# Performance work log

Hardware: AMD Instinct MI355X
Metric: run time of the kernel (lower is better)

The kernel has to match this reference:

```python
import jax, jax.numpy as jnp
import numpy as np


def setup_inputs() -> dict:
    key = jax.random.key(0)
    kq, kk, kv = jax.random.split(key, 3)
    B, S, D = 4, 4096, 128
    q = jax.random.normal(kq, (B, S, D), dtype=jnp.float32)
    k = jax.random.normal(kk, (B, S, D), dtype=jnp.float32)
    v = jax.random.normal(kv, (B, S, D), dtype=jnp.float32)
    return {"q": q, "k": k, "v": v}


def reference(q, k, v):
    # naive scaled dot-product attention: softmax(q k^T / sqrt(d)) v
    scale = 1.0 / jnp.sqrt(jnp.asarray(q.shape[-1], q.dtype))
    scores = jnp.einsum("bsd,btd->bst", q, k) * scale  # [B,S,S]
    probs = jax.nn.softmax(scores, axis=-1)
    out = jnp.einsum("bst,btd->bsd", probs, v)  # [B,S,Dv]
    return out
```

## Files before the change

kernel.cpp:

```cpp
#include <hip/hip_runtime.h>
#include <cmath>
#include <cstdint>

typedef __attribute__((ext_vector_type(8))) __bf16 bf16x8;
typedef __attribute__((ext_vector_type(16))) float f32x16;
typedef unsigned int u32;
typedef unsigned short u16;

constexpr int Bn = 4, Sn = 4096, Dn = 128;
constexpr int OSTR = 132;
constexpr float SCL2E = 0.08838834764831845f * 1.4426950408889634f;

#if __has_builtin(__builtin_amdgcn_exp2f)
#define EXP2F(x) __builtin_amdgcn_exp2f(x)
#else
#define EXP2F(x) exp2f(x)
#endif

__device__ __forceinline__ u32 pk2(float a, float b) {
  u32 r;
  asm("v_cvt_pk_bf16_f32 %0, %1, %2" : "=v"(r) : "v"(a), "v"(b));
  return r;
}

__device__ __forceinline__ void pl32swap(u32& a, u32& b) {
  asm("v_permlane32_swap_b32 %0, %1" : "+v"(a), "+v"(b));
}

__device__ __forceinline__ void gload_lds16(const void* g, void* l) {
  __builtin_amdgcn_global_load_lds(
      (const __attribute__((address_space(1))) u32*)g,
      (__attribute__((address_space(3))) u32*)l, 16, 0, 0);
}

__launch_bounds__(256)
__global__ void prep_kv(const float* __restrict__ Kg, const float* __restrict__ Vg,
                        u16* __restrict__ Kf, u16* __restrict__ Vf) {
  __shared__ float Tl[64 * 132];
  const int kt = blockIdx.x, kind = blockIdx.y, b = blockIdx.z;
  const int tid = threadIdx.x;
  const size_t tileBase = ((size_t)b * 64 + kt) * 1024;
  const float* src = (kind == 0 ? Kg : Vg) + ((size_t)b * Sn + kt * 64) * Dn;

  #pragma unroll
  for (int r = 0; r < 8; ++r) {
    const int idx = tid + r * 256;
    const int row = idx >> 5, col = (idx & 31) * 4;
    float4 v = *(const float4*)(src + (size_t)row * Dn + col);
    *(float4*)(Tl + row * 132 + col) = v;
  }
  __syncthreads();
  if (kind == 0) {
    #pragma unroll
    for (int r = 0; r < 4; ++r) {
      const int g = tid + r * 256;
      const int c = g & 31, h = (g >> 5) & 1, tile = (g >> 6) & 1, kc = g >> 7;
      const float* s = Tl + (tile * 32 + c) * 132 + kc * 16 + h * 8;
      float4 f0 = *(const float4*)(s);
      float4 f1 = *(const float4*)(s + 4);
      uint4 o;
      o.x = pk2(f0.x, f0.y); o.y = pk2(f0.z, f0.w);
      o.z = pk2(f1.x, f1.y); o.w = pk2(f1.z, f1.w);
      *(uint4*)(Kf + (tileBase + g) * 8) = o;
    }
  } else {
    #pragma unroll
    for (int r = 0; r < 4; ++r) {
      const int g = tid + r * 256;
      const int c = g & 31, h = (g >> 5) & 1, nt = (g >> 6) & 3, kc2 = g >> 8;
      const int key0 = kc2 * 16 + h * 8, dcol = nt * 32 + c;
      float x[8];
      #pragma unroll
      for (int j = 0; j < 8; ++j) x[j] = Tl[(key0 + j) * 132 + dcol];
      uint4 o;
      o.x = pk2(x[0], x[1]); o.y = pk2(x[2], x[3]);
      o.z = pk2(x[4], x[5]); o.w = pk2(x[6], x[7]);
      *(uint4*)(Vf + (tileBase + g) * 8) = o;
    }
  }
}

__launch_bounds__(512)
__global__ void attn_tile(const float* __restrict__ qg, const u16* __restrict__ Kf,
                          const u16* __restrict__ Vf, float* __restrict__ Of,
                          float* __restrict__ lw) {
  __shared__ __align__(16) u16 kv[3][16384];

  const int tid = threadIdx.x;
  const int w = tid >> 6, lane = tid & 63;
  const int c = lane & 31, h = lane >> 5;
  const int bks = blockIdx.x & 15, qg2 = blockIdx.x >> 4;
  const int b = bks >> 2, ks = bks & 3;
  const int q0 = qg2 * 256 + w * 32;

  const u16* Kb = Kf + ((size_t)b * 64 + ks * 16) * 8192;
  const u16* Vb = Vf + ((size_t)b * 64 + ks * 16) * 8192;

  bf16x8 qf[8];
  {
    const float* Qr = qg + ((size_t)b * Sn + q0 + c) * Dn;
    #pragma unroll
    for (int kc = 0; kc < 8; ++kc) {
      float4 f0 = *(const float4*)(Qr + kc * 16 + h * 8);
      float4 f1 = *(const float4*)(Qr + kc * 16 + h * 8 + 4);
      uint4 t;
      t.x = pk2(f0.x * SCL2E, f0.y * SCL2E);
      t.y = pk2(f0.z * SCL2E, f0.w * SCL2E);
      t.z = pk2(f1.x * SCL2E, f1.y * SCL2E);
      t.w = pk2(f1.z * SCL2E, f1.w * SCL2E);
      qf[kc] = __builtin_bit_cast(bf16x8, t);
    }
  }

  f32x16 accO[4];
  #pragma unroll
  for (int nt = 0; nt < 4; ++nt)
    #pragma unroll
    for (int r = 0; r < 16; ++r) accO[nt][r] = 0.f;
  float l_i = 0.f;

  u16 *A = &kv[0][0], *B = &kv[1][0], *C = &kv[2][0];

#define STAGE(dst, t_) do {                                                    \
    const u16* kt_ = Kb + (size_t)(t_) * 8192;                                 \
    const u16* vt_ = Vb + (size_t)(t_) * 8192;                                 \
    gload_lds16(kt_ + tid * 8, (dst) + tid * 8);                               \
    gload_lds16(kt_ + 4096 + tid * 8, (dst) + 4096 + tid * 8);                 \
    gload_lds16(vt_ + tid * 8, (dst) + 8192 + tid * 8);                        \
    gload_lds16(vt_ + 4096 + tid * 8, (dst) + 12288 + tid * 8);                \
  } while (0)

  STAGE(A, 0);
  STAGE(B, 1);
  __syncthreads();

  f32x16 sA0, sA1, sB0, sB1;
  {
    #pragma unroll
    for (int r = 0; r < 16; ++r) { sA0[r] = 0.f; sA1[r] = 0.f; }
    __builtin_amdgcn_s_setprio(1);
    #pragma unroll
    for (int kc = 0; kc < 8; ++kc) {
      uint4 a0 = *(const uint4*)(A + (size_t)((kc * 4 + 0 + h) * 32 + c) * 8);
      uint4 a1 = *(const uint4*)(A + (size_t)((kc * 4 + 2 + h) * 32 + c) * 8);
      sA0 = __builtin_amdgcn_mfma_f32_32x32x16_bf16(__builtin_bit_cast(bf16x8, a0), qf[kc], sA0, 0, 0, 0);
      sA1 = __builtin_amdgcn_mfma_f32_32x32x16_bf16(__builtin_bit_cast(bf16x8, a1), qf[kc], sA1, 0, 0, 0);
    }
    __builtin_amdgcn_s_setprio(0);
  }

#define REGION(t_, cur0, cur1, nx0, nx1) do {                                  \
    if ((t_) + 2 < 16) STAGE(C, (t_) + 2);                                     \
    float rs0 = 0.f, rs1 = 0.f;                                                \
    if ((t_) + 1 < 16) {                                                       \
      _Pragma("unroll")                                                        \
      for (int r = 0; r < 16; ++r) { (nx0)[r] = 0.f; (nx1)[r] = 0.f; }         \
      _Pragma("unroll")                                                        \
      for (int kc = 0; kc < 8; ++kc) {                                         \
        uint4 a0 = *(const uint4*)(B + (size_t)((kc * 4 + 0 + h) * 32 + c) * 8); \
        uint4 a1 = *(const uint4*)(B + (size_t)((kc * 4 + 2 + h) * 32 + c) * 8); \
        (nx0) = __builtin_amdgcn_mfma_f32_32x32x16_bf16(__builtin_bit_cast(bf16x8, a0), qf[kc], (nx0), 0, 0, 0); \
        (nx1) = __builtin_amdgcn_mfma_f32_32x32x16_bf16(__builtin_bit_cast(bf16x8, a1), qf[kc], (nx1), 0, 0, 0); \
        float e0 = EXP2F((cur0)[2 * kc]);     rs0 += e0; (cur0)[2 * kc] = e0;     \
        float e1 = EXP2F((cur0)[2 * kc + 1]); rs0 += e1; (cur0)[2 * kc + 1] = e1; \
        float e2 = EXP2F((cur1)[2 * kc]);     rs1 += e2; (cur1)[2 * kc] = e2;     \
        float e3 = EXP2F((cur1)[2 * kc + 1]); rs1 += e3; (cur1)[2 * kc + 1] = e3; \
      }                                                                        \
    } else {                                                                   \
      _Pragma("unroll")                                                        \
      for (int r = 0; r < 16; ++r) {                                           \
        float e0 = EXP2F((cur0)[r]); rs0 += e0; (cur0)[r] = e0;                \
        float e1 = EXP2F((cur1)[r]); rs1 += e1; (cur1)[r] = e1;                \
      }                                                                        \
    }                                                                          \
    l_i += rs0 + rs1;                                                          \
    u32 p0_[8], p1_[8];                                                        \
    _Pragma("unroll")                                                          \
    for (int i_ = 0; i_ < 8; ++i_) {                                           \
      p0_[i_] = pk2((cur0)[2 * i_], (cur0)[2 * i_ + 1]);                       \
      p1_[i_] = pk2((cur1)[2 * i_], (cur1)[2 * i_ + 1]);                       \
    }                                                                          \
    __builtin_amdgcn_s_setprio(1);                                             \
    _Pragma("unroll")                                                          \
    for (int kc2 = 0; kc2 < 4; ++kc2) {                                        \
      const int bb = (kc2 & 1) * 4;                                            \
      u32 x0 = (kc2 < 2) ? p0_[bb] : p1_[bb];                                  \
      u32 x1 = (kc2 < 2) ? p0_[bb + 1] : p1_[bb + 1];                          \
      u32 x2 = (kc2 < 2) ? p0_[bb + 2] : p1_[bb + 2];                          \
      u32 x3 = (kc2 < 2) ? p0_[bb + 3] : p1_[bb + 3];                          \
      pl32swap(x0, x2);                                                        \
      pl32swap(x1, x3);                                                        \
      uint4 afi; afi.x = x0; afi.y = x1; afi.z = x2; afi.w = x3;               \
      bf16x8 af = __builtin_bit_cast(bf16x8, afi);                             \
      _Pragma("unroll")                                                        \
      for (int nt = 0; nt < 4; ++nt) {                                         \
        uint4 av = *(const uint4*)(A + 8192 + (size_t)((kc2 * 8 + nt * 2 + h) * 32 + c) * 8); \
        accO[nt] = __builtin_amdgcn_mfma_f32_32x32x16_bf16(__builtin_bit_cast(bf16x8, av), af, accO[nt], 0, 0, 0); \
      }                                                                        \
    }                                                                          \
    __builtin_amdgcn_s_setprio(0);                                             \
    __syncthreads();                                                           \
    { u16* tmp_ = A; A = B; B = C; C = tmp_; }                                 \
  } while (0)

  #pragma unroll 1
  for (int i = 0; i < 8; ++i) {
    REGION(2 * i, sA0, sA1, sB0, sB1);
    REGION(2 * i + 1, sB0, sB1, sA0, sA1);
  }
#undef REGION
#undef STAGE

  l_i += __shfl_xor(l_i, 32);
  const size_t rowbase = (size_t)ks * 16384 + (size_t)b * 4096 + q0;
  if (h == 0) lw[rowbase + c] = l_i;
  float* op = Of + (rowbase + c) * 128;
  #pragma unroll
  for (int nt = 0; nt < 4; ++nt)
    #pragma unroll
    for (int rq = 0; rq < 4; ++rq) {
      float4 wv = {accO[nt][4 * rq + 0], accO[nt][4 * rq + 1],
                   accO[nt][4 * rq + 2], accO[nt][4 * rq + 3]};
      *(float4*)(op + nt * 32 + rq * 8 + 4 * h) = wv;
    }
}

__launch_bounds__(256)
__global__ void combine(const float* __restrict__ Of, const float* __restrict__ lw,
                        float* __restrict__ Og) {
  const int gid = blockIdx.x * 256 + threadIdx.x;
  const int row = gid >> 4;
  const int d0 = (gid & 15) * 8;
  float ls = 0.f;
  #pragma unroll
  for (int k2 = 0; k2 < 4; ++k2) ls += lw[(size_t)k2 * 16384 + row];
  const float inv = 1.f / ls;
  float a[8] = {0.f, 0.f, 0.f, 0.f, 0.f, 0.f, 0.f, 0.f};
  #pragma unroll
  for (int k2 = 0; k2 < 4; ++k2) {
    const float* p = Of + ((size_t)k2 * 16384 + row) * 128 + d0;
    float4 v0 = *(const float4*)(p);
    float4 v1 = *(const float4*)(p + 4);
    a[0] += v0.x; a[1] += v0.y; a[2] += v0.z; a[3] += v0.w;
    a[4] += v1.x; a[5] += v1.y; a[6] += v1.z; a[7] += v1.w;
  }
  float* op = Og + (size_t)row * 128 + d0;
  float4 o0 = {a[0] * inv, a[1] * inv, a[2] * inv, a[3] * inv};
  float4 o1 = {a[4] * inv, a[5] * inv, a[6] * inv, a[7] * inv};
  *(float4*)(op) = o0;
  *(float4*)(op + 4) = o1;
}

__launch_bounds__(256, 2)
__global__ void attn_legacy(const float* __restrict__ qg, const u16* __restrict__ Kf,
                            const u16* __restrict__ Vf, float* __restrict__ Og) {
  __shared__ __align__(16) unsigned char lds[68608];
  float* Oc = (float*)lds;
  float* ml = (float*)(lds + 67584);

  const int tid = threadIdx.x;
  const int kp = tid >> 6, lane = tid & 63;
  const int c = lane & 31, h = lane >> 5;
  const int b = blockIdx.x & 3;
  const int q0 = (blockIdx.x >> 2) * 32;

  const u16* Kb = Kf + ((size_t)b * 64) * 1024 * 8;
  const u16* Vb = Vf + ((size_t)b * 64) * 1024 * 8;

  bf16x8 qf[8];
  {
    const float* Qr = qg + ((size_t)b * Sn + q0 + c) * Dn;
    #pragma unroll
    for (int kc = 0; kc < 8; ++kc) {
      float4 f0 = *(const float4*)(Qr + kc * 16 + h * 8);
      float4 f1 = *(const float4*)(Qr + kc * 16 + h * 8 + 4);
      uint4 t;
      t.x = pk2(f0.x * SCL2E, f0.y * SCL2E);
      t.y = pk2(f0.z * SCL2E, f0.w * SCL2E);
      t.z = pk2(f1.x * SCL2E, f1.y * SCL2E);
      t.w = pk2(f1.z * SCL2E, f1.w * SCL2E);
      qf[kc] = __builtin_bit_cast(bf16x8, t);
    }
  }

  f32x16 accO[4];
  #pragma unroll
  for (int nt = 0; nt < 4; ++nt)
    #pragma unroll
    for (int r = 0; r < 16; ++r) accO[nt][r] = 0.f;
  float l_i = 0.f;

  #pragma unroll 1
  for (int t8 = 0; t8 < 16; ++t8) {
    const int kt = kp * 16 + t8;
    const u16* Kt = Kb + (size_t)kt * 8192;
    const u16* Vt = Vb + (size_t)kt * 8192;

    uint4 ka[8], kb[8];
    #pragma unroll
    for (int kc = 0; kc < 4; ++kc) {
      ka[2 * kc + 0] = *(const uint4*)(Kt + (size_t)((kc * 4 + 0 + h) * 32 + c) * 8);
      ka[2 * kc + 1] = *(const uint4*)(Kt + (size_t)((kc * 4 + 2 + h) * 32 + c) * 8);
    }
    #pragma unroll
    for (int kc = 4; kc < 8; ++kc) {
      kb[2 * (kc - 4) + 0] = *(const uint4*)(Kt + (size_t)((kc * 4 + 0 + h) * 32 + c) * 8);
      kb[2 * (kc - 4) + 1] = *(const uint4*)(Kt + (size_t)((kc * 4 + 2 + h) * 32 + c) * 8);
    }

    f32x16 sa0, sa1;
    #pragma unroll
    for (int r = 0; r < 16; ++r) { sa0[r] = 0.f; sa1[r] = 0.f; }
    #pragma unroll
    for (int kc = 0; kc < 4; ++kc) {
      sa0 = __builtin_amdgcn_mfma_f32_32x32x16_bf16(__builtin_bit_cast(bf16x8, ka[2 * kc + 0]), qf[kc], sa0, 0, 0, 0);
      sa1 = __builtin_amdgcn_mfma_f32_32x32x16_bf16(__builtin_bit_cast(bf16x8, ka[2 * kc + 1]), qf[kc], sa1, 0, 0, 0);
    }
    uint4 va[8];
    #pragma unroll
    for (int kc2 = 0; kc2 < 2; ++kc2)
      #pragma unroll
      for (int nt = 0; nt < 4; ++nt)
        va[kc2 * 4 + nt] = *(const uint4*)(Vt + (size_t)((kc2 * 8 + nt * 2 + h) * 32 + c) * 8);
    #pragma unroll
    for (int kc = 4; kc < 8; ++kc) {
      sa0 = __builtin_amdgcn_mfma_f32_32x32x16_bf16(__builtin_bit_cast(bf16x8, kb[2 * (kc - 4) + 0]), qf[kc], sa0, 0, 0, 0);
      sa1 = __builtin_amdgcn_mfma_f32_32x32x16_bf16(__builtin_bit_cast(bf16x8, kb[2 * (kc - 4) + 1]), qf[kc], sa1, 0, 0, 0);
    }
    uint4 vb[8];
    #pragma unroll
    for (int kc2 = 2; kc2 < 4; ++kc2)
      #pragma unroll
      for (int nt = 0; nt < 4; ++nt)
        vb[(kc2 - 2) * 4 + nt] = *(const uint4*)(Vt + (size_t)((kc2 * 8 + nt * 2 + h) * 32 + c) * 8);

    float rs0 = 0.f, rs1 = 0.f;
    #pragma unroll
    for (int r = 0; r < 16; ++r) { sa0[r] = exp2f(sa0[r]); rs0 += sa0[r]; }
    #pragma unroll
    for (int r = 0; r < 16; ++r) { sa1[r] = exp2f(sa1[r]); rs1 += sa1[r]; }
    l_i += rs0 + rs1;

    u32 pk2v[2][8];
    #pragma unroll
    for (int i = 0; i < 8; ++i) {
      pk2v[0][i] = pk2(sa0[2 * i], sa0[2 * i + 1]);
      pk2v[1][i] = pk2(sa1[2 * i], sa1[2 * i + 1]);
    }

    #pragma unroll
    for (int kc2 = 0; kc2 < 4; ++kc2) {
      const int t = kc2 >> 1;
      const int bb = (kc2 & 1) * 4;
      u32 x0 = pk2v[t][bb], x1 = pk2v[t][bb + 1], x2 = pk2v[t][bb + 2], x3 = pk2v[t][bb + 3];
      pl32swap(x0, x2);
      pl32swap(x1, x3);
      uint4 afi; afi.x = x0; afi.y = x1; afi.z = x2; afi.w = x3;
      bf16x8 af = __builtin_bit_cast(bf16x8, afi);
      const uint4* vsrc = (kc2 < 2) ? &va[kc2 * 4] : &vb[(kc2 - 2) * 4];
      #pragma unroll
      for (int nt = 0; nt < 4; ++nt) {
        accO[nt] = __builtin_amdgcn_mfma_f32_32x32x16_bf16(__builtin_bit_cast(bf16x8, vsrc[nt]), af, accO[nt], 0, 0, 0);
      }
    }
  }

  l_i += __shfl_xor(l_i, 32);
  __syncthreads();
  {
    float* od = Oc + (size_t)(kp * 32) * OSTR;
    #pragma unroll
    for (int nt = 0; nt < 4; ++nt)
      #pragma unroll
      for (int r = 0; r < 16; ++r) {
        const int dr = (r & 3) + 8 * (r >> 2) + 4 * h;
        od[c * OSTR + nt * 32 + dr] = accO[nt][r];
      }
    if (h == 0) ml[kp * 32 + c] = l_i;
  }
  __syncthreads();
  {
    const int row = tid >> 3;
    const int d0 = (tid & 7) * 16;
    float lsum = 0.f;
    #pragma unroll
    for (int k2 = 0; k2 < 4; ++k2) lsum += ml[k2 * 32 + row];
    const float inv = 1.f / lsum;
    float4 acc[4];
    #pragma unroll
    for (int j = 0; j < 4; ++j) acc[j] = float4{0.f, 0.f, 0.f, 0.f};
    #pragma unroll
    for (int k2 = 0; k2 < 4; ++k2) {
      const float* oc = Oc + (size_t)(k2 * 32 + row) * OSTR + d0;
      #pragma unroll
      for (int j = 0; j < 4; ++j) {
        float4 vv = *(const float4*)(oc + 4 * j);
        acc[j].x += vv.x; acc[j].y += vv.y;
        acc[j].z += vv.z; acc[j].w += vv.w;
      }
    }
    float* op = Og + ((size_t)b * Sn + q0 + row) * Dn + d0;
    #pragma unroll
    for (int j = 0; j < 4; ++j) {
      float4 o = {acc[j].x * inv, acc[j].y * inv, acc[j].z * inv, acc[j].w * inv};
      *(float4*)(op + 4 * j) = o;
    }
  }
}

extern "C" void kernel_launch(void* const* d_in, const int* in_sizes, int n_in,
                              void* d_out, int out_size, void* d_ws, size_t ws_size,
                              hipStream_t stream) {
  const float* q = (const float*)d_in[0];
  const float* k = (const float*)d_in[1];
  const float* v = (const float*)d_in[2];
  float* out = (float*)d_out;
  const size_t N = (size_t)Bn * Sn * Dn;
  u16* Kf = (u16*)d_ws;
  u16* Vf = Kf + N;
  float* Of = (float*)(Vf + N);
  float* lwp = Of + 4 * N;
  const size_t need = 4 * N + 4 * N * sizeof(float) + 4 * (size_t)Bn * Sn * sizeof(float);

  prep_kv<<<dim3(Sn / 64, 2, Bn), dim3(256), 0, stream>>>(k, v, Kf, Vf);
  if (ws_size >= need) {
    attn_tile<<<dim3(256), dim3(512), 0, stream>>>(q, Kf, Vf, Of, lwp);
    combine<<<dim3(1024), dim3(256), 0, stream>>>(Of, lwp, out);
  } else {
    attn_legacy<<<dim3((Sn / 32) * Bn), dim3(256), 0, stream>>>(q, Kf, Vf, out);
  }
}
```

Before: 121.3 us.

## Interleave next-tile QK^T MFMAs with current PV MFMAs instead of exp

Moves the next tile's QK^T MFMA chain out of the exp loop and interleaves it, alternating one instruction at a time, with the current tile's PV MFMAs. The exp computation now runs alone before the matmuls. The aim is to keep independent accumulator chains in flight back-to-back so MFMA dependency stalls are hidden. In exchange, exp no longer overlaps with matrix work, and more operands are live at once, which may raise register pressure.

Result: slower. 141.6 us (+16.8%).

```diff
diff --git a/kernel.cpp b/kernel.cpp
--- a/kernel.cpp
+++ b/kernel.cpp
@@ -152,26 +152,10 @@
 #define REGION(t_, cur0, cur1, nx0, nx1) do {                                  \
     if ((t_) + 2 < 16) STAGE(C, (t_) + 2);                                     \
     float rs0 = 0.f, rs1 = 0.f;                                                \
-    if ((t_) + 1 < 16) {                                                       \
-      _Pragma("unroll")                                                        \
-      for (int r = 0; r < 16; ++r) { (nx0)[r] = 0.f; (nx1)[r] = 0.f; }         \
-      _Pragma("unroll")                                                        \
-      for (int kc = 0; kc < 8; ++kc) {                                         \
-        uint4 a0 = *(const uint4*)(B + (size_t)((kc * 4 + 0 + h) * 32 + c) * 8); \
-        uint4 a1 = *(const uint4*)(B + (size_t)((kc * 4 + 2 + h) * 32 + c) * 8); \
-        (nx0) = __builtin_amdgcn_mfma_f32_32x32x16_bf16(__builtin_bit_cast(bf16x8, a0), qf[kc], (nx0), 0, 0, 0); \
-        (nx1) = __builtin_amdgcn_mfma_f32_32x32x16_bf16(__builtin_bit_cast(bf16x8, a1), qf[kc], (nx1), 0, 0, 0); \
-        float e0 = EXP2F((cur0)[2 * kc]);     rs0 += e0; (cur0)[2 * kc] = e0;     \
-        float e1 = EXP2F((cur0)[2 * kc + 1]); rs0 += e1; (cur0)[2 * kc + 1] = e1; \
-        float e2 = EXP2F((cur1)[2 * kc]);     rs1 += e2; (cur1)[2 * kc] = e2;     \
-        float e3 = EXP2F((cur1)[2 * kc + 1]); rs1 += e3; (cur1)[2 * kc + 1] = e3; \
-      }                                                                        \
-    } else {                                                                   \
-      _Pragma("unroll")                                                        \
-      for (int r = 0; r < 16; ++r) {                                           \
-        float e0 = EXP2F((cur0)[r]); rs0 += e0; (cur0)[r] = e0;                \
-        float e1 = EXP2F((cur1)[r]); rs1 += e1; (cur1)[r] = e1;                \
-      }                                                                        \
+    _Pragma("unroll")                                                          \
+    for (int r = 0; r < 16; ++r) {                                             \
+      float e0 = EXP2F((cur0)[r]); rs0 += e0; (cur0)[r] = e0;                  \
+      float e1 = EXP2F((cur1)[r]); rs1 += e1; (cur1)[r] = e1;                  \
     }                                                                          \
     l_i += rs0 + rs1;                                                          \
     u32 p0_[8], p1_[8];                                                        \
@@ -181,21 +165,55 @@
       p1_[i_] = pk2((cur1)[2 * i_], (cur1)[2 * i_ + 1]);                       \
     }                                                                          \
     __builtin_amdgcn_s_setprio(1);                                             \
-    _Pragma("unroll")                                                          \
-    for (int kc2 = 0; kc2 < 4; ++kc2) {                                        \
-      const int bb = (kc2 & 1) * 4;                                            \
-      u32 x0 = (kc2 < 2) ? p0_[bb] : p1_[bb];                                  \
-      u32 x1 = (kc2 < 2) ? p0_[bb + 1] : p1_[bb + 1];                          \
-      u32 x2 = (kc2 < 2) ? p0_[bb + 2] : p1_[bb + 2];                          \
-      u32 x3 = (kc2 < 2) ? p0_[bb + 3] : p1_[bb + 3];                          \
-      pl32swap(x0, x2);                                                        \
-      pl32swap(x1, x3);                                                        \
-      uint4 afi; afi.x = x0; afi.y = x1; afi.z = x2; afi.w = x3;               \
-      bf16x8 af = __builtin_bit_cast(bf16x8, afi);                             \
+    if ((t_) + 1 < 16) {                                                       \
       _Pragma("unroll")                                                        \
-      for (int nt = 0; nt < 4; ++nt) {                                         \
-        uint4 av = *(const uint4*)(A + 8192 + (size_t)((kc2 * 8 + nt * 2 + h) * 32 + c) * 8); \
-        accO[nt] = __builtin_amdgcn_mfma_f32_32x32x16_bf16(__builtin_bit_cast(bf16x8, av), af, accO[nt], 0, 0, 0); \
+      for (int r = 0; r < 16; ++r) { (nx0)[r] = 0.f; (nx1)[r] = 0.f; }         \
+      _Pragma("unroll")                                                        \
+      for (int kc2 = 0; kc2 < 4; ++kc2) {                                      \
+        const int bb = (kc2 & 1) * 4;                                          \
+        u32 x0 = (kc2 < 2) ? p0_[bb] : p1_[bb];                                \
+        u32 x1 = (kc2 < 2) ? p0_[bb + 1] : p1_[bb + 1];                        \
+        u32 x2 = (kc2 < 2) ? p0_[bb + 2] : p1_[bb + 2];                        \
+        u32 x3 = (kc2 < 2) ? p0_[bb + 3] : p1_[bb + 3];                        \
+        pl32swap(x0, x2);                                                      \
+        pl32swap(x1, x3);                                                      \
+        uint4 afi; afi.x = x0; afi.y = x1; afi.z = x2; afi.w = x3;             \
+        bf16x8 af = __builtin_bit_cast(bf16x8, afi);                           \
+        const int kqa = 2 * kc2, kqb = 2 * kc2 + 1;                            \
+        uint4 qa0 = *(const uint4*)(B + (size_t)((kqa * 4 + 0 + h) * 32 + c) * 8); \
+        uint4 qa1 = *(const uint4*)(B + (size_t)((kqa * 4 + 2 + h) * 32 + c) * 8); \
+        uint4 qb0 = *(const uint4*)(B + (size_t)((kqb * 4 + 0 + h) * 32 + c) * 8); \
+        uint4 qb1 = *(const uint4*)(B + (size_t)((kqb * 4 + 2 + h) * 32 + c) * 8); \
+        uint4 av0 = *(const uint4*)(A + 8192 + (size_t)((kc2 * 8 + 0 * 2 + h) * 32 + c) * 8); \
+        uint4 av1 = *(const uint4*)(A + 8192 + (size_t)((kc2 * 8 + 1 * 2 + h) * 32 + c) * 8); \
+        uint4 av2 = *(const uint4*)(A + 8192 + (size_t)((kc2 * 8 + 2 * 2 + h) * 32 + c) * 8); \
+        uint4 av3 = *(const uint4*)(A + 8192 + (size_t)((kc2 * 8 + 3 * 2 + h) * 32 + c) * 8); \
+        (nx0) = __builtin_amdgcn_mfma_f32_32x32x16_bf16(__builtin_bit_cast(bf16x8, qa0), qf[kqa], (nx0), 0, 0, 0); \
+        accO[0] = __builtin_amdgcn_mfma_f32_32x32x16_bf16(__builtin_bit_cast(bf16x8, av0), af, accO[0], 0, 0, 0);  \
+        (nx1) = __builtin_amdgcn_mfma_f32_32x32x16_bf16(__builtin_bit_cast(bf16x8, qa1), qf[kqa], (nx1), 0, 0, 0); \
+        accO[1] = __builtin_amdgcn_mfma_f32_32x32x16_bf16(__builtin_bit_cast(bf16x8, av1), af, accO[1], 0, 0, 0);  \
+        (nx0) = __builtin_amdgcn_mfma_f32_32x32x16_bf16(__builtin_bit_cast(bf16x8, qb0), qf[kqb], (nx0), 0, 0, 0); \
+        accO[2] = __builtin_amdgcn_mfma_f32_32x32x16_bf16(__builtin_bit_cast(bf16x8, av2), af, accO[2], 0, 0, 0);  \
+        (nx1) = __builtin_amdgcn_mfma_f32_32x32x16_bf16(__builtin_bit_cast(bf16x8, qb1), qf[kqb], (nx1), 0, 0, 0); \
+        accO[3] = __builtin_amdgcn_mfma_f32_32x32x16_bf16(__builtin_bit_cast(bf16x8, av3), af, accO[3], 0, 0, 0);  \
+      }                                                                        \
+    } else {                                                                   \
+      _Pragma("unroll")                                                        \
+      for (int kc2 = 0; kc2 < 4; ++kc2) {                                      \
+        const int bb = (kc2 & 1) * 4;                                          \
+        u32 x0 = (kc2 < 2) ? p0_[bb] : p1_[bb];                                \
+        u32 x1 = (kc2 < 2) ? p0_[bb + 1] : p1_[bb + 1];                        \
+        u32 x2 = (kc2 < 2) ? p0_[bb + 2] : p1_[bb + 2];                        \
+        u32 x3 = (kc2 < 2) ? p0_[bb + 3] : p1_[bb + 3];                        \
+        pl32swap(x0, x2);                                                      \
+        pl32swap(x1, x3);                                                      \
+        uint4 afi; afi.x = x0; afi.y = x1; afi.z = x2; afi.w = x3;             \
+        bf16x8 af = __builtin_bit_cast(bf16x8, afi);                           \
+        _Pragma("unroll")                                                      \
+        for (int nt = 0; nt < 4; ++nt) {                                       \
+          uint4 av = *(const uint4*)(A + 8192 + (size_t)((kc2 * 8 + nt * 2 + h) * 32 + c) * 8); \
+          accO[nt] = __builtin_amdgcn_mfma_f32_32x32x16_bf16(__builtin_bit_cast(bf16x8, av), af, accO[nt], 0, 0, 0); \
+        }                                                                      \
       }                                                                        \
     }                                                                          \
     __builtin_amdgcn_s_setprio(0);                                             \
```
